# Optimization experiments

Measured on AMD Instinct MI355X. Metric: run time of the kernel, lower is better.

## Reference

```python
import jax, jax.numpy as jnp
import numpy as np

G1 = 8      # channel groups
G2 = 16     # spatial blocks per side
C1, C2 = 128, 64
H1 = W1 = 128
H2 = W2 = 256
BS1 = H1 // G2   # 8  -> 64 elems per x1 block
BS2 = H2 // G2   # 16 -> 256 elems per x2 block
BN_EPS = 1e-5


def setup_inputs() -> dict:
    key = jax.random.key(0)
    ks = jax.random.split(key, 16)
    B = 4
    c1g, c2g = C1 // G1, C2 // G1          # 16, 8
    inp = {
        "x1": jax.random.normal(ks[0], (B, C1, H1, W1), jnp.float32),
        "x2": jax.random.normal(ks[1], (B, C2, H2, W2), jnp.float32),
        # Conv1: conv1d k=1, C1//G1 -> C1//2//G1  (16 -> 8)
        "w_c1": jax.random.normal(ks[2], (c1g // 2, c1g), jnp.float32) * 0.1,
        "b_c1": jnp.zeros((c1g // 2,), jnp.float32),
        # Conv2: conv1d k=1, C2//G1 -> C2//G1  (8 -> 8)
        "w_c2": jax.random.normal(ks[3], (c2g, c2g), jnp.float32) * 0.1,
        "b_c2": jnp.zeros((c2g,), jnp.float32),
        # conv1 / conv2: 1x1 conv2d to 1 channel
        "w_p1": jax.random.normal(ks[4], (C1,), jnp.float32) * 0.1,
        "b_p1": jnp.zeros((), jnp.float32),
        "w_p2": jax.random.normal(ks[5], (C2,), jnp.float32) * 0.1,
        "b_p2": jnp.zeros((), jnp.float32),
        # SpatialAttention linear: 64 -> 256 (torch weight layout [out, in])
        "w_lin": jax.random.normal(ks[6], (BS2 * BS2, BS1 * BS1), jnp.float32) * 0.1,
        "b_lin": jnp.zeros((BS2 * BS2,), jnp.float32),
        # convbnrelu: 1x1 conv C2->C2 + BN (eval mode, running stats mean=0 var=1)
        "w_f": jax.random.normal(ks[7], (C2, C2), jnp.float32) * 0.05,
        "b_f": jnp.zeros((C2,), jnp.float32),
        "bn_gamma": jnp.ones((C2,), jnp.float32),
        "bn_beta": jnp.zeros((C2,), jnp.float32),
    }
    return inp


def reference(x1, x2, w_c1, b_c1, w_c2, b_c2, w_p1, b_p1, w_p2, b_p2,
              w_lin, b_lin, w_f, b_f, bn_gamma, bn_beta):
    B = x1.shape[0]
    c1g, c2g = C1 // G1, C2 // G1

    # ---- grouped channel attention (vectorized over the 8 groups) ----
    gap1 = x1.reshape(B, G1, c1g, H1 * W1).mean(-1)           # [B,g,16]
    gap2 = x2.reshape(B, G1, c2g, H2 * W2).mean(-1)           # [B,g,8]
    mlp1 = jax.nn.relu(jnp.einsum('oc,bgc->bgo', w_c1, gap1) + b_c1)  # [B,g,8]
    mlp2 = jax.nn.relu(jnp.einsum('oc,bgc->bgo', w_c2, gap2) + b_c2)  # [B,g,8]
    sem = jnp.einsum('bgo,bgp->bgop', mlp1, mlp2)             # [B,g,8,8]
    cw_logits = jnp.einsum('bgop,bgp->bgo', sem, mlp2)        # [B,g,8]
    cw = jax.nn.softmax(cw_logits, axis=-1)                   # softmax over channel dim
    sem_x2 = (x2.reshape(B, G1, c2g, H2, W2) * cw[..., None, None]
              ).reshape(B, C2, H2, W2)

    # ---- block-wise spatial attention (vectorized over 16x16 blocks) ----
    nb = G2 * G2
    x1b = x1.reshape(B, C1, G2, BS1, G2, BS1).transpose(0, 2, 4, 1, 3, 5)
    x1b = x1b.reshape(B, nb, C1, BS1, BS1)
    x2b = x2.reshape(B, C2, G2, BS2, G2, BS2).transpose(0, 2, 4, 1, 3, 5)
    x2b = x2b.reshape(B, nb, C2, BS2, BS2)

    pos1 = (jnp.einsum('c,bncij->bnij', w_p1, x1b) + b_p1).reshape(B, nb, BS1 * BS1)
    pos2 = (jnp.einsum('c,bncij->bnij', w_p2, x2b) + b_p2).reshape(B, nb, BS2 * BS2)

    x1t = jnp.einsum('oc,bnc->bno', w_lin, pos1) + b_lin      # [B,nb,256]
    # bmm(x2^T, x1t) is an outer product since both are rank-1 per block
    scores = pos2[..., :, None] * x1t[..., None, :]           # [B,nb,256,256]
    aw = jax.nn.softmax(scores, axis=-1)
    weighted = jnp.einsum('bnq,bnqk->bnk', pos2, aw)          # [B,nb,256]
    # torch.cat(dim=2).view(B,1,H2,W2): raw row-major flatten of block outputs
    spa = weighted.reshape(B, 1, H2, W2)

    # ---- fuse: 1x1 conv + BN(eval) + ReLU ----
    pre = sem_x2 + spa
    conv = jnp.einsum('oc,bchw->bohw', w_f, pre) + b_f[:, None, None]
    bn = conv / jnp.sqrt(jnp.float32(1.0 + BN_EPS)) * bn_gamma[:, None, None] \
         + bn_beta[:, None, None]
    return jax.nn.relu(bn)
```

## Files before the change

### kernel.cpp

```cpp
#include <hip/hip_runtime.h>


#define GAP_OFF  0
#define P2_OFF   768
#define P3_OFF   832
#define WF2T_OFF 896
#define POS1_OFF 17280
#define POS2_OFF 82816
#define SPA_OFF  344960

__global__ __launch_bounds__(256) void k_fuse(const float* __restrict__ x1,
                                              const float* __restrict__ x2,
                                              const float* __restrict__ w_p1,
                                              const float* __restrict__ b_p1,
                                              const float* __restrict__ w_p2,
                                              const float* __restrict__ b_p2,
                                              float* __restrict__ ws) {
  __shared__ float gbuf[128 * 65];
  __shared__ float pbuf[1024];
  int blk = blockIdx.x, t = threadIdx.x;
  int wv = t >> 6, ln = t & 63;
  if (blk < 256) {
    int b = blk >> 6;
    int px0 = (blk & 63) << 8;
    const float* xb = x1 + ((size_t)b << 21) + px0 + (ln << 2);
    float4 pacc; pacc.x = pacc.y = pacc.z = pacc.w = 0.f;
    float gs[32];
#pragma unroll
    for (int i = 0; i < 32; ++i) {
      int c = (i << 2) + wv;
      float4 v = *(const float4*)(xb + ((size_t)c << 14));
      float wc = w_p1[c];
      pacc.x = fmaf(wc, v.x, pacc.x); pacc.y = fmaf(wc, v.y, pacc.y);
      pacc.z = fmaf(wc, v.z, pacc.z); pacc.w = fmaf(wc, v.w, pacc.w);
      gs[i] = (v.x + v.y) + (v.z + v.w);
    }
#pragma unroll
    for (int i = 0; i < 32; ++i) gbuf[((wv << 5) + i) * 65 + ln] = gs[i];
    *(float4*)&pbuf[(wv << 8) + (ln << 2)] = pacc;
    __syncthreads();
    if (t < 128) {
      int w2 = t >> 5, i2 = t & 31;
      int c = (i2 << 2) + w2;
      const float* gp = &gbuf[t * 65];
      float s0 = 0.f, s1 = 0.f, s2 = 0.f, s3 = 0.f;
#pragma unroll
      for (int k = 0; k < 64; k += 4) { s0 += gp[k]; s1 += gp[k+1]; s2 += gp[k+2]; s3 += gp[k+3]; }
      atomicAdd(&ws[GAP_OFF + b * 128 + c], (s0 + s1) + (s2 + s3));
    }
    float s = (pbuf[t] + pbuf[256 + t]) + (pbuf[512 + t] + pbuf[768 + t]) + b_p1[0];
    int p = px0 + t, h = p >> 7, w0 = p & 127;
    int n = ((h >> 3) << 4) + (w0 >> 3);
    ws[POS1_OFF + ((b * 256 + n) << 6) + ((h & 7) << 3) + (w0 & 7)] = s;
  } else {
    int j = blk - 256;
    int b = j >> 8;
    int row = j & 255;
    const float* xb = x2 + ((size_t)b << 22) + (row << 8) + (ln << 2);
    float4 pacc; pacc.x = pacc.y = pacc.z = pacc.w = 0.f;
    float gs[16];
#pragma unroll
    for (int i = 0; i < 16; ++i) {
      int c = (i << 2) + wv;
      float4 v = *(const float4*)(xb + ((size_t)c << 16));
      float wc = w_p2[c];
      pacc.x = fmaf(wc, v.x, pacc.x); pacc.y = fmaf(wc, v.y, pacc.y);
      pacc.z = fmaf(wc, v.z, pacc.z); pacc.w = fmaf(wc, v.w, pacc.w);
      gs[i] = (v.x + v.y) + (v.z + v.w);
    }
#pragma unroll
    for (int i = 0; i < 16; ++i) gbuf[((wv << 4) + i) * 65 + ln] = gs[i];
    *(float4*)&pbuf[(wv << 8) + (ln << 2)] = pacc;
    __syncthreads();
    if (t < 64) {
      int w2 = t >> 4, i2 = t & 15;
      int c = (i2 << 2) + w2;
      const float* gp = &gbuf[t * 65];
      float s0 = 0.f, s1 = 0.f, s2 = 0.f, s3 = 0.f;
#pragma unroll
      for (int k = 0; k < 64; k += 4) { s0 += gp[k]; s1 += gp[k+1]; s2 += gp[k+2]; s3 += gp[k+3]; }
      atomicAdd(&ws[GAP_OFF + 512 + b * 64 + c], (s0 + s1) + (s2 + s3));
    }
    float s = (pbuf[t] + pbuf[256 + t]) + (pbuf[512 + t] + pbuf[768 + t]) + b_p2[0];
    int n = ((row >> 4) << 4) + (t >> 4);
    ws[POS2_OFF + ((b * 256 + n) << 8) + ((row & 15) << 4) + (t & 15)] = s;
  }
}

__global__ __launch_bounds__(256) void k_attn(const float* __restrict__ w_lin,
                                              const float* __restrict__ b_lin,
                                              const float* __restrict__ w_c1,
                                              const float* __restrict__ b_c1,
                                              const float* __restrict__ w_c2,
                                              const float* __restrict__ b_c2,
                                              const float* __restrict__ w_f,
                                              const float* __restrict__ b_f,
                                              const float* __restrict__ gm,
                                              const float* __restrict__ bt,
                                              float* __restrict__ ws) {
  __shared__ float smem[1104];
  int t = threadIdx.x;
  const float kbn = 0.99999500003749969f;
  if (blockIdx.x == 1024) {
    float* g1s = smem;
    float* g2s = smem + 512;
    float* cw_s = smem + 768;
    for (int idx = t; idx < 512; idx += 256) g1s[idx] = ws[GAP_OFF + idx] * (1.f / 16384.f);
    g2s[t] = ws[GAP_OFF + 512 + t] * (1.f / 65536.f);
    __syncthreads();
    if (t < 32) {
      int b = t >> 3, g = t & 7;
      const float* g1 = g1s + b * 128 + g * 16;
      const float* g2 = g2s + b * 64 + g * 8;
      float m1[8], m2[8];
      for (int o = 0; o < 8; ++o) {
        float s = b_c1[o];
        for (int c = 0; c < 16; ++c) s = fmaf(w_c1[o * 16 + c], g1[c], s);
        m1[o] = fmaxf(s, 0.f);
      }
      float ss = 0.f;
      for (int p = 0; p < 8; ++p) {
        float s = b_c2[p];
        for (int c = 0; c < 8; ++c) s = fmaf(w_c2[p * 8 + c], g2[c], s);
        float r = fmaxf(s, 0.f);
        m2[p] = r; ss = fmaf(r, r, ss);
      }
      float lg[8], mx = -1e30f;
      for (int o = 0; o < 8; ++o) { lg[o] = m1[o] * ss; mx = fmaxf(mx, lg[o]); }
      float se = 0.f;
      for (int o = 0; o < 8; ++o) {
        lg[o] = __builtin_amdgcn_exp2f((lg[o] - mx) * 1.44269504088896f);
        se += lg[o];
      }
      float inv = 1.f / se;
      for (int o = 0; o < 8; ++o) cw_s[b * 64 + g * 8 + o] = lg[o] * inv;
    }
    __syncthreads();
    if (t < 64) {
      float s = 0.f;
      for (int c = 0; c < 64; ++c) s += w_f[t * 64 + c];
      float A = kbn * gm[t];
      ws[P2_OFF + t] = s * A;
      ws[P3_OFF + t] = fmaf(b_f[t], A, bt[t]);
    }
    for (int i = t; i < 16384; i += 256) {
      int b = i >> 12, rem = i & 4095;
      int c = rem >> 6, o = rem & 63;
      ws[WF2T_OFF + i] = w_f[o * 64 + c] * cw_s[b * 64 + c] * (kbn * gm[o]);
    }
    return;
  }
  float* P1 = smem;
  float* V  = smem + 64;
  float* A2 = smem + 320;
  float* T  = smem + 576;
  float* rmx = smem + 832;
  float* rmn = smem + 836;
  const float L2E = 1.44269504088896f;
  int bn = blockIdx.x;
  if (t < 64) P1[t] = ws[POS1_OFF + bn * 64 + t];
  float a = ws[POS2_OFF + bn * 256 + t];
  float a2 = a * L2E;
  A2[t] = a2;
  __syncthreads();
  float v = b_lin[t];
  const float* wr = w_lin + t * 64;
#pragma unroll 16
  for (int c = 0; c < 64; ++c) v = fmaf(wr[c], P1[c], v);
  V[t] = v;
  float vmax = v, vmin = v;
#pragma unroll
  for (int m = 32; m; m >>= 1) {
    vmax = fmaxf(vmax, __shfl_xor(vmax, m));
    vmin = fminf(vmin, __shfl_xor(vmin, m));
  }
  if ((t & 63) == 0) { rmx[t >> 6] = vmax; rmn[t >> 6] = vmin; }
  __syncthreads();
  vmax = fmaxf(fmaxf(rmx[0], rmx[1]), fmaxf(rmx[2], rmx[3]));
  vmin = fminf(fminf(rmn[0], rmn[1]), fminf(rmn[2], rmn[3]));
  float m2 = (a2 > 0.f) ? a2 * vmax : a2 * vmin;
  float d0 = 0.f, d1 = 0.f, d2 = 0.f, d3 = 0.f;
#pragma unroll 4
  for (int k = 0; k < 256; k += 4) {
    float4 vv = *(float4*)&V[k];
    d0 += __builtin_amdgcn_exp2f(fmaf(a2, vv.x, -m2));
    d1 += __builtin_amdgcn_exp2f(fmaf(a2, vv.y, -m2));
    d2 += __builtin_amdgcn_exp2f(fmaf(a2, vv.z, -m2));
    d3 += __builtin_amdgcn_exp2f(fmaf(a2, vv.w, -m2));
  }
  float den = (d0 + d1) + (d2 + d3);
  T[t] = (a / den) * __builtin_amdgcn_exp2f(-m2);
  __syncthreads();
  float c0 = 0.f, c1 = 0.f, c2 = 0.f, c3 = 0.f;
#pragma unroll 4
  for (int q = 0; q < 256; q += 4) {
    float4 aq = *(float4*)&A2[q];
    float4 tq = *(float4*)&T[q];
    c0 = fmaf(tq.x, __builtin_amdgcn_exp2f(aq.x * v), c0);
    c1 = fmaf(tq.y, __builtin_amdgcn_exp2f(aq.y * v), c1);
    c2 = fmaf(tq.z, __builtin_amdgcn_exp2f(aq.z * v), c2);
    c3 = fmaf(tq.w, __builtin_amdgcn_exp2f(aq.w * v), c3);
  }
  ws[SPA_OFF + bn * 256 + t] = (c0 + c1) + (c2 + c3);
}

__global__ __launch_bounds__(256) void k_final(const float* __restrict__ x2,
                                               const float* __restrict__ ws,
                                               float* __restrict__ out) {
  __shared__ float Xt[64 * 256];
  __shared__ float Mt[64 * 64];
  int t = threadIdx.x;
  int blk = blockIdx.x;
  int b = blk >> 8;
  int p0 = (blk & 255) << 8;
  const float* xg = x2 + ((size_t)b << 22) + p0;
#pragma unroll
  for (int i = 0; i < 16; ++i) {
    int f4 = i * 256 + t;
    int c = f4 >> 6, col = (f4 & 63) << 2;
    float4 v = *(const float4*)(xg + ((size_t)c << 16) + col);
    *(float4*)&Xt[c * 256 + col] = v;
  }
  const float* mg = ws + WF2T_OFF + (b << 12);
#pragma unroll
  for (int i = 0; i < 4; ++i) {
    int f4 = i * 256 + t;
    *(float4*)&Mt[f4 << 2] = *(const float4*)(mg + ((size_t)f4 << 2));
  }
  __syncthreads();
  int og = (t >> 5) << 3;
  int pA = (t & 31) << 2;
  int pB = pA + 128;
  float acc[8][8];
#pragma unroll
  for (int i = 0; i < 8; ++i)
#pragma unroll
    for (int j = 0; j < 8; ++j) acc[i][j] = 0.f;
#pragma unroll 4
  for (int c = 0; c < 64; ++c) {
    float4 xa = *(float4*)&Xt[c * 256 + pA];
    float4 xb = *(float4*)&Xt[c * 256 + pB];
    float4 ma = *(float4*)&Mt[(c << 6) + og];
    float4 mb = *(float4*)&Mt[(c << 6) + og + 4];
    float xs[8] = {xa.x, xa.y, xa.z, xa.w, xb.x, xb.y, xb.z, xb.w};
    float ms[8] = {ma.x, ma.y, ma.z, ma.w, mb.x, mb.y, mb.z, mb.w};
#pragma unroll
    for (int i = 0; i < 8; ++i)
#pragma unroll
      for (int j = 0; j < 8; ++j)
        acc[i][j] = fmaf(ms[i], xs[j], acc[i][j]);
  }
  const float* sp = ws + SPA_OFF + (b << 16) + p0;
  float4 sa = *(const float4*)(sp + pA);
  float4 sb = *(const float4*)(sp + pB);
  float spa[8] = {sa.x, sa.y, sa.z, sa.w, sb.x, sb.y, sb.z, sb.w};
  float* outp = out + ((size_t)b << 22) + p0;
#pragma unroll
  for (int i = 0; i < 8; ++i) {
    int o = og + i;
    float p2 = ws[P2_OFF + o];
    float p3 = ws[P3_OFF + o];
    float r[8];
#pragma unroll
    for (int j = 0; j < 8; ++j)
      r[j] = fmaxf(fmaf(spa[j], p2, acc[i][j] + p3), 0.f);
    float4 r0; r0.x = r[0]; r0.y = r[1]; r0.z = r[2]; r0.w = r[3];
    float4 r1; r1.x = r[4]; r1.y = r[5]; r1.z = r[6]; r1.w = r[7];
    float* po = outp + ((size_t)o << 16);
    *(float4*)(po + pA) = r0;
    *(float4*)(po + pB) = r1;
  }
}

extern "C" void kernel_launch(void* const* d_in, const int* in_sizes, int n_in,
                              void* d_out, int out_size, void* d_ws, size_t ws_size,
                              hipStream_t stream) {
  const float* x1   = (const float*)d_in[0];
  const float* x2   = (const float*)d_in[1];
  const float* w_c1 = (const float*)d_in[2];
  const float* b_c1 = (const float*)d_in[3];
  const float* w_c2 = (const float*)d_in[4];
  const float* b_c2 = (const float*)d_in[5];
  const float* w_p1 = (const float*)d_in[6];
  const float* b_p1 = (const float*)d_in[7];
  const float* w_p2 = (const float*)d_in[8];
  const float* b_p2 = (const float*)d_in[9];
  const float* w_lin= (const float*)d_in[10];
  const float* b_lin= (const float*)d_in[11];
  const float* w_f  = (const float*)d_in[12];
  const float* b_f  = (const float*)d_in[13];
  const float* gmm  = (const float*)d_in[14];
  const float* btt  = (const float*)d_in[15];
  float* ws  = (float*)d_ws;
  float* out = (float*)d_out;

  hipMemsetAsync(ws, 0, 768 * sizeof(float), stream);
  hipLaunchKernelGGL(k_fuse,  dim3(1280), dim3(256), 0, stream, x1, x2, w_p1, b_p1, w_p2, b_p2, ws);
  hipLaunchKernelGGL(k_attn,  dim3(1025), dim3(256), 0, stream, w_lin, b_lin,
                     w_c1, b_c1, w_c2, b_c2, w_f, b_f, gmm, btt, ws);
  hipLaunchKernelGGL(k_final, dim3(1024), dim3(256), 0, stream, x2, ws, out);
}
```

Measured before the change: 222.1 us.

## Merge attention and final fuse kernels into one, recomputing channel weights per block

Fuses k_attn and k_final into one kernel, k_mrg. Each block computes its spatial-attention output in shared memory and then applies the 1x1 conv, BN and ReLU for the same 256-pixel tile. The per-batch channel-attention weights and the fused conv matrix are now recomputed in every block rather than by one dedicated block, and x2 is read from global memory directly inside the conv loop with no shared-memory staging. This removes a kernel launch and the workspace round trip for spa and the weight matrix. The cost is redundant small compute per block and uncoalesced-style per-thread global loads of x2 in the inner loop.

```diff
diff --git a/kernel.cpp b/kernel.cpp
--- a/kernel.cpp
+++ b/kernel.cpp
@@ -2,12 +2,8 @@
 
 
 #define GAP_OFF  0
-#define P2_OFF   768
-#define P3_OFF   832
-#define WF2T_OFF 896
-#define POS1_OFF 17280
-#define POS2_OFF 82816
-#define SPA_OFF  344960
+#define POS1_OFF 768
+#define POS2_OFF 66304
 
 __global__ __launch_bounds__(256) void k_fuse(const float* __restrict__ x1,
                                               const float* __restrict__ x2,
@@ -87,82 +83,37 @@
   }
 }
 
-__global__ __launch_bounds__(256) void k_attn(const float* __restrict__ w_lin,
-                                              const float* __restrict__ b_lin,
-                                              const float* __restrict__ w_c1,
-                                              const float* __restrict__ b_c1,
-                                              const float* __restrict__ w_c2,
-                                              const float* __restrict__ b_c2,
-                                              const float* __restrict__ w_f,
-                                              const float* __restrict__ b_f,
-                                              const float* __restrict__ gm,
-                                              const float* __restrict__ bt,
-                                              float* __restrict__ ws) {
-  __shared__ float smem[1104];
+__global__ __launch_bounds__(256) void k_mrg(const float* __restrict__ x2,
+                                             const float* __restrict__ w_lin,
+                                             const float* __restrict__ b_lin,
+                                             const float* __restrict__ w_c1,
+                                             const float* __restrict__ b_c1,
+                                             const float* __restrict__ w_c2,
+                                             const float* __restrict__ b_c2,
+                                             const float* __restrict__ w_f,
+                                             const float* __restrict__ b_f,
+                                             const float* __restrict__ gm,
+                                             const float* __restrict__ bt,
+                                             const float* __restrict__ ws,
+                                             float* __restrict__ out) {
+  __shared__ float Mt[4096];
+  __shared__ float P1[64], V[256], A2[256], T[256], spa_s[256];
+  __shared__ float g1s[128], g2s[64], cw_l[64], p2s[64], p3s[64];
+  __shared__ float rmx[4], rmn[4];
+  const float L2E = 1.44269504088896f;
+  const float kbn = 0.99999500003749969f;
   int t = threadIdx.x;
-  const float kbn = 0.99999500003749969f;
-  if (blockIdx.x == 1024) {
-    float* g1s = smem;
-    float* g2s = smem + 512;
-    float* cw_s = smem + 768;
-    for (int idx = t; idx < 512; idx += 256) g1s[idx] = ws[GAP_OFF + idx] * (1.f / 16384.f);
-    g2s[t] = ws[GAP_OFF + 512 + t] * (1.f / 65536.f);
-    __syncthreads();
-    if (t < 32) {
-      int b = t >> 3, g = t & 7;
-      const float* g1 = g1s + b * 128 + g * 16;
-      const float* g2 = g2s + b * 64 + g * 8;
-      float m1[8], m2[8];
-      for (int o = 0; o < 8; ++o) {
-        float s = b_c1[o];
-        for (int c = 0; c < 16; ++c) s = fmaf(w_c1[o * 16 + c], g1[c], s);
-        m1[o] = fmaxf(s, 0.f);
-      }
-      float ss = 0.f;
-      for (int p = 0; p < 8; ++p) {
-        float s = b_c2[p];
-        for (int c = 0; c < 8; ++c) s = fmaf(w_c2[p * 8 + c], g2[c], s);
-        float r = fmaxf(s, 0.f);
-        m2[p] = r; ss = fmaf(r, r, ss);
-      }
-      float lg[8], mx = -1e30f;
-      for (int o = 0; o < 8; ++o) { lg[o] = m1[o] * ss; mx = fmaxf(mx, lg[o]); }
-      float se = 0.f;
-      for (int o = 0; o < 8; ++o) {
-        lg[o] = __builtin_amdgcn_exp2f((lg[o] - mx) * 1.44269504088896f);
-        se += lg[o];
-      }
-      float inv = 1.f / se;
-      for (int o = 0; o < 8; ++o) cw_s[b * 64 + g * 8 + o] = lg[o] * inv;
-    }
-    __syncthreads();
-    if (t < 64) {
-      float s = 0.f;
-      for (int c = 0; c < 64; ++c) s += w_f[t * 64 + c];
-      float A = kbn * gm[t];
-      ws[P2_OFF + t] = s * A;
-      ws[P3_OFF + t] = fmaf(b_f[t], A, bt[t]);
-    }
-    for (int i = t; i < 16384; i += 256) {
-      int b = i >> 12, rem = i & 4095;
-      int c = rem >> 6, o = rem & 63;
-      ws[WF2T_OFF + i] = w_f[o * 64 + c] * cw_s[b * 64 + c] * (kbn * gm[o]);
-    }
-    return;
-  }
-  float* P1 = smem;
-  float* V  = smem + 64;
-  float* A2 = smem + 320;
-  float* T  = smem + 576;
-  float* rmx = smem + 832;
-  float* rmn = smem + 836;
-  const float L2E = 1.44269504088896f;
-  int bn = blockIdx.x;
-  if (t < 64) P1[t] = ws[POS1_OFF + bn * 64 + t];
-  float a = ws[POS2_OFF + bn * 256 + t];
+  int blk = blockIdx.x;
+  int b = blk >> 8, n = blk & 255;
+
+  if (t < 128) g1s[t] = ws[GAP_OFF + b * 128 + t] * (1.f / 16384.f);
+  if (t < 64)  g2s[t] = ws[GAP_OFF + 512 + b * 64 + t] * (1.f / 65536.f);
+  if (t < 64)  P1[t] = ws[POS1_OFF + blk * 64 + t];
+  float a = ws[POS2_OFF + blk * 256 + t];
   float a2 = a * L2E;
   A2[t] = a2;
   __syncthreads();
+
   float v = b_lin[t];
   const float* wr = w_lin + t * 64;
 #pragma unroll 16
@@ -175,7 +126,35 @@
     vmin = fminf(vmin, __shfl_xor(vmin, m));
   }
   if ((t & 63) == 0) { rmx[t >> 6] = vmax; rmn[t >> 6] = vmin; }
-  __syncthreads();
+  if (t < 8) {
+    int g = t;
+    const float* g1 = g1s + g * 16;
+    const float* g2 = g2s + g * 8;
+    float m1[8];
+    for (int o = 0; o < 8; ++o) {
+      float s = b_c1[o];
+      for (int c = 0; c < 16; ++c) s = fmaf(w_c1[o * 16 + c], g1[c], s);
+      m1[o] = fmaxf(s, 0.f);
+    }
+    float ss = 0.f;
+    for (int p = 0; p < 8; ++p) {
+      float s = b_c2[p];
+      for (int c = 0; c < 8; ++c) s = fmaf(w_c2[p * 8 + c], g2[c], s);
+      float r = fmaxf(s, 0.f);
+      ss = fmaf(r, r, ss);
+    }
+    float lg[8], mx = -1e30f;
+    for (int o = 0; o < 8; ++o) { lg[o] = m1[o] * ss; mx = fmaxf(mx, lg[o]); }
+    float se = 0.f;
+    for (int o = 0; o < 8; ++o) {
+      lg[o] = __builtin_amdgcn_exp2f((lg[o] - mx) * L2E);
+      se += lg[o];
+    }
+    float inv = 1.f / se;
+    for (int o = 0; o < 8; ++o) cw_l[g * 8 + o] = lg[o] * inv;
+  }
+  __syncthreads();
+
   vmax = fmaxf(fmaxf(rmx[0], rmx[1]), fmaxf(rmx[2], rmx[3]));
   vmin = fminf(fminf(rmn[0], rmn[1]), fminf(rmn[2], rmn[3]));
   float m2 = (a2 > 0.f) ? a2 * vmax : a2 * vmin;
@@ -190,7 +169,20 @@
   }
   float den = (d0 + d1) + (d2 + d3);
   T[t] = (a / den) * __builtin_amdgcn_exp2f(-m2);
-  __syncthreads();
+  if (t < 64) {
+    const float4* wrow = (const float4*)(w_f + t * 64);
+    float s0 = 0.f, s1 = 0.f, s2 = 0.f, s3 = 0.f;
+#pragma unroll
+    for (int k = 0; k < 16; ++k) {
+      float4 wv = wrow[k];
+      s0 += wv.x; s1 += wv.y; s2 += wv.z; s3 += wv.w;
+    }
+    float A = kbn * gm[t];
+    p2s[t] = ((s0 + s1) + (s2 + s3)) * A;
+    p3s[t] = fmaf(b_f[t], A, bt[t]);
+  }
+  __syncthreads();
+
   float c0 = 0.f, c1 = 0.f, c2 = 0.f, c3 = 0.f;
 #pragma unroll 4
   for (int q = 0; q < 256; q += 4) {
@@ -201,36 +193,19 @@
     c2 = fmaf(tq.z, __builtin_amdgcn_exp2f(aq.z * v), c2);
     c3 = fmaf(tq.w, __builtin_amdgcn_exp2f(aq.w * v), c3);
   }
-  ws[SPA_OFF + bn * 256 + t] = (c0 + c1) + (c2 + c3);
-}
-
-__global__ __launch_bounds__(256) void k_final(const float* __restrict__ x2,
-                                               const float* __restrict__ ws,
-                                               float* __restrict__ out) {
-  __shared__ float Xt[64 * 256];
-  __shared__ float Mt[64 * 64];
-  int t = threadIdx.x;
-  int blk = blockIdx.x;
-  int b = blk >> 8;
-  int p0 = (blk & 255) << 8;
-  const float* xg = x2 + ((size_t)b << 22) + p0;
+  spa_s[t] = (c0 + c1) + (c2 + c3);
 #pragma unroll
   for (int i = 0; i < 16; ++i) {
-    int f4 = i * 256 + t;
-    int c = f4 >> 6, col = (f4 & 63) << 2;
-    float4 v = *(const float4*)(xg + ((size_t)c << 16) + col);
-    *(float4*)&Xt[c * 256 + col] = v;
-  }
-  const float* mg = ws + WF2T_OFF + (b << 12);
-#pragma unroll
-  for (int i = 0; i < 4; ++i) {
-    int f4 = i * 256 + t;
-    *(float4*)&Mt[f4 << 2] = *(const float4*)(mg + ((size_t)f4 << 2));
-  }
-  __syncthreads();
+    int idx = i * 256 + t;
+    int c = idx >> 6, o = idx & 63;
+    Mt[idx] = w_f[o * 64 + c] * cw_l[c] * (kbn * gm[o]);
+  }
+  __syncthreads();
+
   int og = (t >> 5) << 3;
   int pA = (t & 31) << 2;
   int pB = pA + 128;
+  const float* xg = x2 + ((size_t)b << 22) + (n << 8);
   float acc[8][8];
 #pragma unroll
   for (int i = 0; i < 8; ++i)
@@ -238,8 +213,8 @@
     for (int j = 0; j < 8; ++j) acc[i][j] = 0.f;
 #pragma unroll 4
   for (int c = 0; c < 64; ++c) {
-    float4 xa = *(float4*)&Xt[c * 256 + pA];
-    float4 xb = *(float4*)&Xt[c * 256 + pB];
+    float4 xa = *(const float4*)(xg + ((size_t)c << 16) + pA);
+    float4 xb = *(const float4*)(xg + ((size_t)c << 16) + pB);
     float4 ma = *(float4*)&Mt[(c << 6) + og];
     float4 mb = *(float4*)&Mt[(c << 6) + og + 4];
     float xs[8] = {xa.x, xa.y, xa.z, xa.w, xb.x, xb.y, xb.z, xb.w};
@@ -250,16 +225,15 @@
       for (int j = 0; j < 8; ++j)
         acc[i][j] = fmaf(ms[i], xs[j], acc[i][j]);
   }
-  const float* sp = ws + SPA_OFF + (b << 16) + p0;
-  float4 sa = *(const float4*)(sp + pA);
-  float4 sb = *(const float4*)(sp + pB);
-  float spa[8] = {sa.x, sa.y, sa.z, sa.w, sb.x, sb.y, sb.z, sb.w};
-  float* outp = out + ((size_t)b << 22) + p0;
+  float spa[8];
+#pragma unroll
+  for (int j = 0; j < 4; ++j) { spa[j] = spa_s[pA + j]; spa[4 + j] = spa_s[pB + j]; }
+  float* outp = out + ((size_t)b << 22) + (n << 8);
 #pragma unroll
   for (int i = 0; i < 8; ++i) {
     int o = og + i;
-    float p2 = ws[P2_OFF + o];
-    float p3 = ws[P3_OFF + o];
+    float p2 = p2s[o];
+    float p3 = p3s[o];
     float r[8];
 #pragma unroll
     for (int j = 0; j < 8; ++j)
@@ -295,8 +269,7 @@
   float* out = (float*)d_out;
 
   hipMemsetAsync(ws, 0, 768 * sizeof(float), stream);
-  hipLaunchKernelGGL(k_fuse,  dim3(1280), dim3(256), 0, stream, x1, x2, w_p1, b_p1, w_p2, b_p2, ws);
-  hipLaunchKernelGGL(k_attn,  dim3(1025), dim3(256), 0, stream, w_lin, b_lin,
-                     w_c1, b_c1, w_c2, b_c2, w_f, b_f, gmm, btt, ws);
-  hipLaunchKernelGGL(k_final, dim3(1024), dim3(256), 0, stream, x2, ws, out);
+  hipLaunchKernelGGL(k_fuse, dim3(1280), dim3(256), 0, stream, x1, x2, w_p1, b_p1, w_p2, b_p2, ws);
+  hipLaunchKernelGGL(k_mrg,  dim3(1024), dim3(256), 0, stream, x2, w_lin, b_lin,
+                     w_c1, b_c1, w_c2, b_c2, w_f, b_f, gmm, btt, ws, out);
 }
```

Result: no change. 222.0 us (-0.0%).
